# Kernel optimization log

Measured on AMD Instinct MI355X. Metric: run time of the kernel, lower is better.

The kernel has to match this reference:

```python
import jax, jax.numpy as jnp
import numpy as np

N_NODES = 100000
N_EDGES = 3200000
D_NODE = 16
D_EDGE = 8
D_HIDDEN = 16


def setup_inputs() -> dict:
    key = jax.random.key(0)
    ks = jax.random.split(key, 8)
    node_features = jax.random.normal(ks[0], (N_NODES, D_NODE), dtype=jnp.float32)
    edge_attr_e3nn = jax.random.normal(ks[1], (N_EDGES, D_EDGE), dtype=jnp.float32)
    node_attr_scalar_raw = jax.random.normal(ks[2], (N_NODES, 1), dtype=jnp.float32)
    W_msg_tp = jax.random.normal(ks[3], (D_NODE, D_EDGE, D_HIDDEN), dtype=jnp.float32)
    W_msg_lin = jax.random.normal(ks[4], (D_HIDDEN, D_HIDDEN), dtype=jnp.float32)
    W_upd_tp = jax.random.normal(ks[5], (D_NODE, D_HIDDEN, D_HIDDEN), dtype=jnp.float32)
    W_upd_lin = jax.random.normal(ks[6], (D_HIDDEN, D_NODE), dtype=jnp.float32)
    edge_index = jax.random.randint(ks[7], (2, N_EDGES), 0, N_NODES, dtype=jnp.int64)
    return {
        "node_features": node_features,
        "edge_attr_e3nn": edge_attr_e3nn,
        "node_attr_scalar_raw": node_attr_scalar_raw,
        "W_msg_tp": W_msg_tp,
        "W_msg_lin": W_msg_lin,
        "W_upd_tp": W_upd_tp,
        "W_upd_lin": W_upd_lin,
        "edge_index": edge_index,
    }


def reference(node_features, edge_attr_e3nn, node_attr_scalar_raw,
              W_msg_tp, W_msg_lin, W_upd_tp, W_upd_lin, edge_index):
    n_nodes = node_features.shape[0]
    row = edge_index[0]  # destination (aggregation target)
    col = edge_index[1]  # source (gathered neighbor)

    # fan-in normalizations (e3nn FullyConnectedTensorProduct / Linear convention)
    norm_msg_tp = 1.0 / np.float32(np.sqrt(D_NODE * D_EDGE))
    norm_upd_tp = 1.0 / np.float32(np.sqrt(D_NODE * D_HIDDEN))
    norm_lin = 1.0 / np.float32(np.sqrt(D_HIDDEN))

    # --- message step: gather -> bilinear TP -> gate -> linear ---
    x_j = node_features[col]                                   # [E, D_node]
    m = jnp.einsum('ei,ej,ijh->eh', x_j, edge_attr_e3nn, W_msg_tp) * norm_msg_tp
    m = jax.nn.silu(m)                                         # gate nonlinearity
    m = (m @ W_msg_lin) * norm_lin                             # [E, D_hidden]

    # --- scatter-sum aggregation into nodes ---
    agg = jax.ops.segment_sum(m, row, num_segments=n_nodes)    # [N, D_hidden]

    # --- update step: bilinear TP -> gate -> linear -> residual ---
    u = jnp.einsum('ni,nh,ihk->nk', node_features, agg, W_upd_tp) * norm_upd_tp
    u = jax.nn.silu(u)
    u = (u @ W_upd_lin) * norm_lin                             # [N, D_node]

    return node_features + u
```

## Files before the change

### kernel.cpp

```cpp
#include <hip/hip_runtime.h>
#include <math.h>

#define N_NODES_C 100000
#define N_EDGES_C 3200000

#define NORM_MSG_TP 0.08838834764831845f
#define NORM_UPD_TP 0.0625f
#define NORM_LIN    0.25f

typedef float f32x4 __attribute__((ext_vector_type(4)));
typedef short bf16x8 __attribute__((ext_vector_type(8)));
typedef int   int4v  __attribute__((ext_vector_type(4)));

__device__ __forceinline__ float silu_f(float v) {
  return v / (1.0f + __expf(-v));
}

__device__ __forceinline__ void atomic_add_hw(float* p, float v) {
  unsafeAtomicAdd(p, v);
}

__device__ __forceinline__ unsigned int bf16_bits(float f) {
  unsigned int b = __float_as_uint(f);
  return (b + 0x7fffu + ((b >> 16) & 1u)) >> 16;
}
__device__ __forceinline__ unsigned int pack_bf16x2(float lo, float hi) {
  return bf16_bits(lo) | (bf16_bits(hi) << 16);
}
__device__ __forceinline__ float unlo(unsigned int w) { return __uint_as_float(w << 16); }
__device__ __forceinline__ float unhi(unsigned int w) { return __uint_as_float(w & 0xffff0000u); }


__global__ __launch_bounds__(256) void zero_ints(int* __restrict__ p, int n) {
  int i = blockIdx.x * 256 + threadIdx.x;
  if (i < n) p[i] = 0;
}

__global__ __launch_bounds__(256) void hist_kernel(
    const int* __restrict__ row, int* __restrict__ cnt) {
  int e = blockIdx.x * 256 + threadIdx.x;
  atomicAdd(&cnt[row[e]], 1);
}

__global__ __launch_bounds__(256) void scan_block(
    const int* __restrict__ cnt, int* __restrict__ off, int* __restrict__ bsum, int n) {
  __shared__ int s[256];
  const int t = threadIdx.x;
  const int i = blockIdx.x * 256 + t;
  const int v = (i < n) ? cnt[i] : 0;
  s[t] = v;
  __syncthreads();
#pragma unroll
  for (int o = 1; o < 256; o <<= 1) {
    int tv = (t >= o) ? s[t - o] : 0;
    __syncthreads();
    s[t] += tv;
    __syncthreads();
  }
  if (i < n) off[i] = s[t] - v;
  if (t == 255) bsum[blockIdx.x] = s[255];
}

__global__ void scan_bsum(int* __restrict__ bsum, int nb) {
  __shared__ int s[512];
  const int t = threadIdx.x;
  const int v = (t < nb) ? bsum[t] : 0;
  s[t] = v;
  __syncthreads();
#pragma unroll
  for (int o = 1; o < 512; o <<= 1) {
    int tv = (t >= o) ? s[t - o] : 0;
    __syncthreads();
    s[t] += tv;
    __syncthreads();
  }
  if (t < nb) bsum[t] = s[t] - v;
}

__global__ __launch_bounds__(256) void scan_add(
    int* __restrict__ off, const int* __restrict__ bsum, int n, int total) {
  int i = blockIdx.x * 256 + threadIdx.x;
  if (i < n) off[i] += bsum[blockIdx.x];
  if (i == 0) off[n] = total;
}


__global__ __launch_bounds__(256) void xcast_kernel(
    const float* __restrict__ x, unsigned short* __restrict__ xb) {
  const int i = blockIdx.x * 256 + threadIdx.x;
  if (i < N_NODES_C * 2) {
    const float4 a = *reinterpret_cast<const float4*>(x + (size_t)i * 8);
    const float4 b = *reinterpret_cast<const float4*>(x + (size_t)i * 8 + 4);
    uint4 w;
    w.x = pack_bf16x2(a.x, a.y); w.y = pack_bf16x2(a.z, a.w);
    w.z = pack_bf16x2(b.x, b.y); w.w = pack_bf16x2(b.z, b.w);
    *reinterpret_cast<uint4*>(xb + (size_t)i * 8) = w;
  }
}


#define CLAIM_TILE(T, CC, PP) do {                                   \
    const int e_ = (T) * 16 + r;                                     \
    if (g == 0) {                                                    \
      CC = eidx[N_EDGES_C + e_];                                     \
      const int rd_ = eidx[e_];                                      \
      PP = off[rd_] + atomicSub(&cnt[rd_], 1) - 1;                   \
    }                                                                \
  } while (0)

#define GATH_TILE(T, CC, XH, F4) do {                                \
    const int e_ = (T) * 16 + r;                                     \
    const int c_ = __shfl(CC, r);                                    \
    if (g < 2) {                                                     \
      XH = *reinterpret_cast<const uint4*>(xb + (size_t)c_ * 16 + g * 8); \
      F4 = *reinterpret_cast<const float4*>(ea + (size_t)e_ * 8 + g * 4); \
    }                                                                \
  } while (0)

__global__ __launch_bounds__(256) void place4_kernel(
    const int*   __restrict__ eidx,
    const float* __restrict__ ea,
    const float* __restrict__ Wtp,
    const int*   __restrict__ off,
    int*         __restrict__ cnt,
    const unsigned short* __restrict__ xb,
    unsigned int* __restrict__ msort)
{
  __shared__ float sm[4][16][20];
  const int lane  = threadIdx.x & 63;
  const int wv    = threadIdx.x >> 6;
  const int r     = lane & 15;
  const int g     = lane >> 4;
  const int gsel  = g >> 1;
  const int ghalf = g & 1;

  bf16x8 bq[4];
#pragma unroll
  for (int q = 0; q < 4; ++q) {
#pragma unroll
    for (int t = 0; t < 8; ++t) {
      const float w = Wtp[(8 * ghalf + t) * 128 + (2 * q + gsel) * 16 + r];
      bq[q][t] = (short)bf16_bits(w);
    }
  }

  const int s = gridDim.x * 4;
  const int wid = blockIdx.x * 4 + wv;
  const int ntiles = N_EDGES_C / 16;

  int cc_a = 0, pp_a = 0, cc_b = 0, pp_b = 0;
  uint4 xh_a; xh_a.x = xh_a.y = xh_a.z = xh_a.w = 0;
  float4 f4_a = make_float4(0.f, 0.f, 0.f, 0.f);

  if (wid < ntiles)     CLAIM_TILE(wid, cc_a, pp_a);
  if (wid + s < ntiles) CLAIM_TILE(wid + s, cc_b, pp_b);
  if (wid < ntiles)     GATH_TILE(wid, cc_a, xh_a, f4_a);

  for (int t = wid; t < ntiles; t += s) {
    int cc_c = 0, pp_c = 0;
    if (t + 2 * s < ntiles) CLAIM_TILE(t + 2 * s, cc_c, pp_c);
    uint4 xh_b; xh_b.x = xh_b.y = xh_b.z = xh_b.w = 0;
    float4 f4_b = make_float4(0.f, 0.f, 0.f, 0.f);
    if (t + s < ntiles) GATH_TILE(t + s, cc_b, xh_b, f4_b);

    uint4 xh;
    xh.x = (unsigned)__shfl((int)xh_a.x, ghalf * 16 + r);
    xh.y = (unsigned)__shfl((int)xh_a.y, ghalf * 16 + r);
    xh.z = (unsigned)__shfl((int)xh_a.z, ghalf * 16 + r);
    xh.w = (unsigned)__shfl((int)xh_a.w, ghalf * 16 + r);
    float xf[8];
    xf[0] = unlo(xh.x); xf[1] = unhi(xh.x);
    xf[2] = unlo(xh.y); xf[3] = unhi(xh.y);
    xf[4] = unlo(xh.z); xf[5] = unhi(xh.z);
    xf[6] = unlo(xh.w); xf[7] = unhi(xh.w);
    const float a0 = __shfl(f4_a.x, r),      a1 = __shfl(f4_a.y, r);
    const float a2 = __shfl(f4_a.z, r),      a3 = __shfl(f4_a.w, r);
    const float b0 = __shfl(f4_a.x, 16 + r), b1 = __shfl(f4_a.y, 16 + r);
    const float b2 = __shfl(f4_a.z, 16 + r), b3 = __shfl(f4_a.w, 16 + r);
    float eq[4];
    eq[0] = gsel ? a1 : a0;  eq[1] = gsel ? a3 : a2;
    eq[2] = gsel ? b1 : b0;  eq[3] = gsel ? b3 : b2;

    f32x4 acc = {0.f, 0.f, 0.f, 0.f};
#pragma unroll
    for (int q = 0; q < 4; ++q) {
      const float e_ = eq[q];
      const unsigned u0 = __float_as_uint(xf[0] * e_) + 0x8000u;
      const unsigned u1 = __float_as_uint(xf[1] * e_) + 0x8000u;
      const unsigned u2 = __float_as_uint(xf[2] * e_) + 0x8000u;
      const unsigned u3 = __float_as_uint(xf[3] * e_) + 0x8000u;
      const unsigned u4 = __float_as_uint(xf[4] * e_) + 0x8000u;
      const unsigned u5 = __float_as_uint(xf[5] * e_) + 0x8000u;
      const unsigned u6 = __float_as_uint(xf[6] * e_) + 0x8000u;
      const unsigned u7 = __float_as_uint(xf[7] * e_) + 0x8000u;
      int4v iv;
      iv.x = (int)__builtin_amdgcn_perm(u1, u0, 0x07060302u);
      iv.y = (int)__builtin_amdgcn_perm(u3, u2, 0x07060302u);
      iv.z = (int)__builtin_amdgcn_perm(u5, u4, 0x07060302u);
      iv.w = (int)__builtin_amdgcn_perm(u7, u6, 0x07060302u);
      union { int4v i; bf16x8 h; } cv; cv.i = iv;
      acc = __builtin_amdgcn_mfma_f32_16x16x32_bf16(cv.h, bq[q], acc, 0, 0, 0);
    }

#pragma unroll
    for (int j2 = 0; j2 < 4; ++j2)
      sm[wv][g * 4 + j2][r] = silu_f(acc[j2] * NORM_MSG_TP);

    asm volatile("s_waitcnt lgkmcnt(0)" ::: "memory");
    __builtin_amdgcn_sched_barrier(0);

    const int rr  = lane >> 2;
    const int wsl = lane & 3;
    const float4 v4 = *reinterpret_cast<const float4*>(&sm[wv][rr][wsl * 4]);
    const int prr = __shfl(pp_a, rr);
    uint2 wout;
    wout.x = pack_bf16x2(v4.x, v4.y);
    wout.y = pack_bf16x2(v4.z, v4.w);
    *reinterpret_cast<uint2*>(&msort[(size_t)prr * 8 + wsl * 2]) = wout;

    pp_a = pp_b; xh_a = xh_b; f4_a = f4_b;
    cc_b = cc_c; pp_b = pp_c;
  }
}


__global__ __launch_bounds__(256) void agg3_kernel(
    const float* __restrict__ Wlin,
    const unsigned int* __restrict__ msort,
    const int*   __restrict__ off,
    float*       __restrict__ agg)
{
  __shared__ float sL[256];
  if (threadIdx.x < 256) sL[threadIdx.x] = Wlin[threadIdx.x];
  __syncthreads();

  const int slane = threadIdx.x & 15;
  const int n = blockIdx.x * 16 + (threadIdx.x >> 4);

  const int off0 = off[n];
  const int off1 = off[n + 1];

  float acc = 0.f;
  for (int p = off0; p < off1; ++p) {
    const unsigned int w = msort[(size_t)p * 8 + (slane >> 1)];
    acc += (slane & 1) ? unhi(w) : unlo(w);
  }

  float a = 0.f;
#pragma unroll
  for (int h = 0; h < 16; ++h) {
    const float v = __shfl(acc, h, 16);
    a = fmaf(v, sL[h * 16 + slane], a);
  }
  agg[(size_t)n * 16 + slane] = a * NORM_LIN;
}


__global__ __launch_bounds__(256) void tbuild_kernel(
    const float* __restrict__ x, const float* __restrict__ Wtp,
    uint4* __restrict__ Tb)
{
  __shared__ float sWT[16 * 132];
  for (int idx = threadIdx.x; idx < 2048; idx += 256) {
    const int i = idx >> 7, j = (idx >> 4) & 7, h = idx & 15;
    sWT[h * 132 + i * 8 + j] = Wtp[idx];
  }
  __syncthreads();

  const int slane = threadIdx.x & 15;
  const int n = blockIdx.x * 16 + (threadIdx.x >> 4);

  float xr[16];
  const float4* xp = reinterpret_cast<const float4*>(x + (size_t)n * 16);
#pragma unroll
  for (int q = 0; q < 4; ++q) {
    float4 v = xp[q];
    xr[q*4+0] = v.x; xr[q*4+1] = v.y; xr[q*4+2] = v.z; xr[q*4+3] = v.w;
  }

  float t[8];
#pragma unroll
  for (int j = 0; j < 8; ++j) t[j] = 0.f;
#pragma unroll
  for (int i = 0; i < 16; ++i) {
    const float xi = xr[i];
    const float4 wa = *reinterpret_cast<const float4*>(&sWT[slane * 132 + i * 8]);
    const float4 wb = *reinterpret_cast<const float4*>(&sWT[slane * 132 + i * 8 + 4]);
    t[0] = fmaf(xi, wa.x, t[0]); t[1] = fmaf(xi, wa.y, t[1]);
    t[2] = fmaf(xi, wa.z, t[2]); t[3] = fmaf(xi, wa.w, t[3]);
    t[4] = fmaf(xi, wb.x, t[4]); t[5] = fmaf(xi, wb.y, t[5]);
    t[6] = fmaf(xi, wb.z, t[6]); t[7] = fmaf(xi, wb.w, t[7]);
  }
  uint4 w;
  w.x = pack_bf16x2(t[0], t[1]);
  w.y = pack_bf16x2(t[2], t[3]);
  w.z = pack_bf16x2(t[4], t[5]);
  w.w = pack_bf16x2(t[6], t[7]);
  Tb[(size_t)n * 16 + slane] = w;
}

__global__ __launch_bounds__(256) void place_kernel(
    const int* __restrict__ eidx, const float* __restrict__ ea,
    const int* __restrict__ off, int* __restrict__ cnt,
    int* __restrict__ colp, uint4* __restrict__ eab) {
  int e = blockIdx.x * 256 + threadIdx.x;
  const int r = eidx[e];
  const int old = atomicSub(&cnt[r], 1);
  const int p = off[r] + old - 1;
  colp[p] = eidx[N_EDGES_C + e];
  const float4* ep = reinterpret_cast<const float4*>(ea + (size_t)e * 8);
  const float4 a = ep[0];
  const float4 b = ep[1];
  uint4 w;
  w.x = pack_bf16x2(a.x, a.y);
  w.y = pack_bf16x2(a.z, a.w);
  w.z = pack_bf16x2(b.x, b.y);
  w.w = pack_bf16x2(b.z, b.w);
  eab[p] = w;
}

__global__ __launch_bounds__(256) void agg2_kernel(
    const float* __restrict__ Wlin, const int* __restrict__ colp,
    const uint4* __restrict__ eab, const uint4* __restrict__ Tb,
    const int* __restrict__ off, float* __restrict__ agg)
{
  __shared__ float sL[256];
  if (threadIdx.x < 256) sL[threadIdx.x] = Wlin[threadIdx.x];
  __syncthreads();

  const int slane = threadIdx.x & 15;
  const int n = blockIdx.x * 16 + (threadIdx.x >> 4);

  const int off0 = off[n];
  const int off1 = off[n + 1];

  float acc = 0.f;
#pragma unroll 2
  for (int p = off0; p < off1; ++p) {
    const int c = colp[p];
    const uint4 tw = Tb[(size_t)c * 16 + slane];
    const uint4 ew = eab[p];
    float m;
    m  = unlo(ew.x) * unlo(tw.x);
    m  = fmaf(unhi(ew.x), unhi(tw.x), m);
    m  = fmaf(unlo(ew.y), unlo(tw.y), m);
    m  = fmaf(unhi(ew.y), unhi(tw.y), m);
    m  = fmaf(unlo(ew.z), unlo(tw.z), m);
    m  = fmaf(unhi(ew.z), unhi(tw.z), m);
    m  = fmaf(unlo(ew.w), unlo(tw.w), m);
    m  = fmaf(unhi(ew.w), unhi(tw.w), m);
    acc += silu_f(m * NORM_MSG_TP);
  }

  float a = 0.f;
#pragma unroll
  for (int h = 0; h < 16; ++h) {
    const float v = __shfl(acc, h, 16);
    a = fmaf(v, sL[h * 16 + slane], a);
  }
  agg[(size_t)n * 16 + slane] = a * NORM_LIN;
}


__global__ __launch_bounds__(256) void node_kernel(
    const float* __restrict__ x, const float* __restrict__ agg,
    const float* __restrict__ Wtp, const float* __restrict__ Wlin,
    float* __restrict__ out)
{
  __shared__ float sW[4096];
  __shared__ float sL[256];
  for (int t = threadIdx.x; t < 4096; t += 256) sW[t] = Wtp[t];
  sL[threadIdx.x] = Wlin[threadIdx.x];
  __syncthreads();

  const long n = (long)blockIdx.x * 256 + threadIdx.x;
  if (n >= N_NODES_C) return;

  float xr[16], ar[16];
  const float4* xp = reinterpret_cast<const float4*>(x + (size_t)n * 16);
  const float4* ap = reinterpret_cast<const float4*>(agg + (size_t)n * 16);
#pragma unroll
  for (int q = 0; q < 4; ++q) {
    float4 v = xp[q];
    xr[q*4+0] = v.x; xr[q*4+1] = v.y; xr[q*4+2] = v.z; xr[q*4+3] = v.w;
    float4 w = ap[q];
    ar[q*4+0] = w.x; ar[q*4+1] = w.y; ar[q*4+2] = w.z; ar[q*4+3] = w.w;
  }
  float u[16];
#pragma unroll
  for (int k = 0; k < 16; ++k) u[k] = 0.f;
#pragma unroll
  for (int i = 0; i < 16; ++i) {
#pragma unroll
    for (int h = 0; h < 16; ++h) {
      const float p = xr[i] * ar[h];
      const float* w = &sW[(i*16 + h) * 16];
#pragma unroll
      for (int k = 0; k < 16; ++k) u[k] = fmaf(p, w[k], u[k]);
    }
  }
  float g[16];
#pragma unroll
  for (int k = 0; k < 16; ++k) g[k] = silu_f(u[k] * NORM_UPD_TP);
  float res[16];
#pragma unroll
  for (int k2 = 0; k2 < 16; ++k2) {
    float a = 0.f;
#pragma unroll
    for (int k = 0; k < 16; ++k) a = fmaf(g[k], sL[k*16 + k2], a);
    res[k2] = xr[k2] + a * NORM_LIN;
  }
  float4* op = reinterpret_cast<float4*>(out + (size_t)n * 16);
#pragma unroll
  for (int q = 0; q < 4; ++q)
    op[q] = make_float4(res[q*4+0], res[q*4+1], res[q*4+2], res[q*4+3]);
}


__global__ void zero_f4(float4* __restrict__ p, int n4) {
  int i = blockIdx.x * blockDim.x + threadIdx.x;
  if (i < n4) p[i] = make_float4(0.f, 0.f, 0.f, 0.f);
}

#define EPT 2
__global__ __launch_bounds__(256) void edge_kernel(
    const float* __restrict__ x, const float* __restrict__ ea,
    const float* __restrict__ Wtp, const float* __restrict__ Wlin,
    const int* __restrict__ eidx, float* __restrict__ agg)
{
  __shared__ float sW[2048];
  __shared__ float sL[256];
  for (int t = threadIdx.x; t < 2048; t += 256) sW[t] = Wtp[t];
  sL[threadIdx.x] = Wlin[threadIdx.x];
  __syncthreads();
  const long e0 = ((long)blockIdx.x * 256 + threadIdx.x) * EPT;
  float xr[EPT][16], er[EPT][8];
  int rw[EPT];
#pragma unroll
  for (int e = 0; e < EPT; ++e) {
    const long ei = e0 + e;
    const int c = eidx[N_EDGES_C + ei];
    rw[e] = eidx[ei];
    const float4* xp = reinterpret_cast<const float4*>(x + (size_t)c * 16);
#pragma unroll
    for (int q = 0; q < 4; ++q) {
      float4 v = xp[q];
      xr[e][q*4+0] = v.x; xr[e][q*4+1] = v.y; xr[e][q*4+2] = v.z; xr[e][q*4+3] = v.w;
    }
    const float4* ep = reinterpret_cast<const float4*>(ea + (size_t)ei * 8);
#pragma unroll
    for (int q = 0; q < 2; ++q) {
      float4 v = ep[q];
      er[e][q*4+0] = v.x; er[e][q*4+1] = v.y; er[e][q*4+2] = v.z; er[e][q*4+3] = v.w;
    }
  }
  float m[EPT][16];
#pragma unroll
  for (int e = 0; e < EPT; ++e)
#pragma unroll
    for (int h = 0; h < 16; ++h) m[e][h] = 0.f;
#pragma unroll
  for (int i = 0; i < 16; ++i) {
#pragma unroll
    for (int j = 0; j < 8; ++j) {
      float p[EPT];
#pragma unroll
      for (int e = 0; e < EPT; ++e) p[e] = xr[e][i] * er[e][j];
      const float* w = &sW[(i*8 + j) * 16];
#pragma unroll
      for (int h = 0; h < 16; ++h) {
        const float wv = w[h];
#pragma unroll
        for (int e = 0; e < EPT; ++e) m[e][h] = fmaf(p[e], wv, m[e][h]);
      }
    }
  }
#pragma unroll
  for (int e = 0; e < EPT; ++e) {
    float g[16];
#pragma unroll
    for (int h = 0; h < 16; ++h) g[h] = silu_f(m[e][h] * NORM_MSG_TP);
    float* ap = agg + (size_t)rw[e] * 16;
#pragma unroll
    for (int h2 = 0; h2 < 16; ++h2) {
      float a = 0.f;
#pragma unroll
      for (int h = 0; h < 16; ++h) a = fmaf(g[h], sL[h*16 + h2], a);
      atomic_add_hw(ap + h2, a * NORM_LIN);
    }
  }
}


extern "C" void kernel_launch(void* const* d_in, const int* in_sizes, int n_in,
                              void* d_out, int out_size, void* d_ws, size_t ws_size,
                              hipStream_t stream) {
  const float* node_features = (const float*)d_in[0];
  const float* edge_attr     = (const float*)d_in[1];
  const float* W_msg_tp      = (const float*)d_in[3];
  const float* W_msg_lin     = (const float*)d_in[4];
  const float* W_upd_tp      = (const float*)d_in[5];
  const float* W_upd_lin     = (const float*)d_in[6];
  const int*   edge_index    = (const int*)d_in[7];
  float* out = (float*)d_out;
  char* ws = (char*)d_ws;

  const int NB_N = (N_NODES_C + 255) / 256;
  const int NB_E = N_EDGES_C / 256;
  const int NB_G = N_NODES_C / 16;

  const size_t A_OFF  = 0;
  const size_t A_CNT  = 400128;
  const size_t A_BSUM = 800256;
  const size_t A_MSORT= 802304;
  const size_t A_XB   = A_MSORT + 102400000;
  const size_t A_AGG  = A_XB + 3200000;
  const size_t A_NEED = A_AGG + 6400000;

  const size_t B_OFF  = 0;
  const size_t B_CNT  = 400128;
  const size_t B_BSUM = 800256;
  const size_t B_COLP = 804352;
  const size_t B_EAB  = B_COLP + 12800000;
  const size_t B_T    = B_EAB + 51200000;
  const size_t B_AGG  = B_T + 25600000;
  const size_t B_NEED = B_AGG + 6400000;

  if (ws_size >= A_NEED) {
    int*   off   = (int*)(ws + A_OFF);
    int*   cnt   = (int*)(ws + A_CNT);
    int*   bsum  = (int*)(ws + A_BSUM);
    unsigned int* msort = (unsigned int*)(ws + A_MSORT);
    unsigned short* xb  = (unsigned short*)(ws + A_XB);
    float* agg   = (float*)(ws + A_AGG);

    hipLaunchKernelGGL(zero_ints, dim3(NB_N), dim3(256), 0, stream, cnt, N_NODES_C);
    hipLaunchKernelGGL(hist_kernel, dim3(NB_E), dim3(256), 0, stream, edge_index, cnt);
    hipLaunchKernelGGL(scan_block, dim3(NB_N), dim3(256), 0, stream,
                       cnt, off, bsum, N_NODES_C);
    hipLaunchKernelGGL(scan_bsum, dim3(1), dim3(512), 0, stream, bsum, NB_N);
    hipLaunchKernelGGL(scan_add, dim3(NB_N), dim3(256), 0, stream,
                       off, bsum, N_NODES_C, N_EDGES_C);
    hipLaunchKernelGGL(xcast_kernel, dim3((N_NODES_C * 2 + 255) / 256), dim3(256),
                       0, stream, node_features, xb);
    hipLaunchKernelGGL(place4_kernel, dim3(2048), dim3(256), 0, stream,
                       edge_index, edge_attr, W_msg_tp, off, cnt, xb, msort);
    hipLaunchKernelGGL(agg3_kernel, dim3(NB_G), dim3(256), 0, stream,
                       W_msg_lin, msort, off, agg);
    hipLaunchKernelGGL(node_kernel, dim3(NB_N), dim3(256), 0, stream,
                       node_features, agg, W_upd_tp, W_upd_lin, out);
  } else if (ws_size >= B_NEED) {
    int*   off  = (int*)(ws + B_OFF);
    int*   cnt  = (int*)(ws + B_CNT);
    int*   bsum = (int*)(ws + B_BSUM);
    int*   colp = (int*)(ws + B_COLP);
    uint4* eab  = (uint4*)(ws + B_EAB);
    uint4* Tb   = (uint4*)(ws + B_T);
    float* agg  = (float*)(ws + B_AGG);

    hipLaunchKernelGGL(zero_ints, dim3(NB_N), dim3(256), 0, stream, cnt, N_NODES_C);
    hipLaunchKernelGGL(hist_kernel, dim3(NB_E), dim3(256), 0, stream, edge_index, cnt);
    hipLaunchKernelGGL(scan_block, dim3(NB_N), dim3(256), 0, stream,
                       cnt, off, bsum, N_NODES_C);
    hipLaunchKernelGGL(scan_bsum, dim3(1), dim3(512), 0, stream, bsum, NB_N);
    hipLaunchKernelGGL(scan_add, dim3(NB_N), dim3(256), 0, stream,
                       off, bsum, N_NODES_C, N_EDGES_C);
    hipLaunchKernelGGL(place_kernel, dim3(NB_E), dim3(256), 0, stream,
                       edge_index, edge_attr, off, cnt, colp, eab);
    hipLaunchKernelGGL(tbuild_kernel, dim3(NB_G), dim3(256), 0, stream,
                       node_features, W_msg_tp, Tb);
    hipLaunchKernelGGL(agg2_kernel, dim3(NB_G), dim3(256), 0, stream,
                       W_msg_lin, colp, eab, Tb, off, agg);
    hipLaunchKernelGGL(node_kernel, dim3(NB_N), dim3(256), 0, stream,
                       node_features, agg, W_upd_tp, W_upd_lin, out);
  } else {
    float* agg = (float*)ws;
    const int n4 = N_NODES_C * 16 / 4;
    hipLaunchKernelGGL(zero_f4, dim3((n4 + 255) / 256), dim3(256), 0, stream,
                       (float4*)agg, n4);
    hipLaunchKernelGGL(edge_kernel, dim3(N_EDGES_C / (256 * EPT)), dim3(256), 0, stream,
                       node_features, edge_attr, W_msg_tp, W_msg_lin, edge_index, agg);
    hipLaunchKernelGGL(node_kernel, dim3(NB_N), dim3(256), 0, stream,
                       node_features, agg, W_upd_tp, W_upd_lin, out);
  }
}
```

Measured before the change: 381.7 us.

## Write messages in edge order and gather via permutation during aggregation

Splits the edge placement out into its own kernel that builds a CSR permutation of edge ids. The message kernel now writes bf16 messages contiguously in edge order instead of scattering them to sorted positions. The aggregation kernel gathers messages indirectly through the permutation, unrolled by four. This swaps scattered 16-byte writes for coalesced writes, at the cost of an extra kernel, a 12.8 MB permutation array, and random reads during aggregation.

```diff
diff --git a/kernel.cpp b/kernel.cpp
--- a/kernel.cpp
+++ b/kernel.cpp
@@ -82,6 +82,15 @@
   int i = blockIdx.x * 256 + threadIdx.x;
   if (i < n) off[i] += bsum[blockIdx.x];
   if (i == 0) off[n] = total;
+}
+
+__global__ __launch_bounds__(256) void placeP_kernel(
+    const int* __restrict__ eidx, const int* __restrict__ off,
+    int* __restrict__ cnt, int* __restrict__ perm) {
+  int e = blockIdx.x * 256 + threadIdx.x;
+  const int r = eidx[e];
+  const int p = off[r] + atomicSub(&cnt[r], 1) - 1;
+  perm[p] = e;
 }
 
 
@@ -99,13 +108,8 @@
 }
 
 
-#define CLAIM_TILE(T, CC, PP) do {                                   \
-    const int e_ = (T) * 16 + r;                                     \
-    if (g == 0) {                                                    \
-      CC = eidx[N_EDGES_C + e_];                                     \
-      const int rd_ = eidx[e_];                                      \
-      PP = off[rd_] + atomicSub(&cnt[rd_], 1) - 1;                   \
-    }                                                                \
+#define COLS_TILE(T, CC) do {                                        \
+    if (g == 0) CC = eidx[N_EDGES_C + (T) * 16 + r];                 \
   } while (0)
 
 #define GATH_TILE(T, CC, XH, F4) do {                                \
@@ -117,14 +121,12 @@
     }                                                                \
   } while (0)
 
-__global__ __launch_bounds__(256) void place4_kernel(
+__global__ __launch_bounds__(256) void msg_kernel(
     const int*   __restrict__ eidx,
     const float* __restrict__ ea,
     const float* __restrict__ Wtp,
-    const int*   __restrict__ off,
-    int*         __restrict__ cnt,
     const unsigned short* __restrict__ xb,
-    unsigned int* __restrict__ msort)
+    unsigned int* __restrict__ msgb)
 {
   __shared__ float sm[4][16][20];
   const int lane  = threadIdx.x & 63;
@@ -148,17 +150,17 @@
   const int wid = blockIdx.x * 4 + wv;
   const int ntiles = N_EDGES_C / 16;
 
-  int cc_a = 0, pp_a = 0, cc_b = 0, pp_b = 0;
+  int cc_a = 0, cc_b = 0;
   uint4 xh_a; xh_a.x = xh_a.y = xh_a.z = xh_a.w = 0;
   float4 f4_a = make_float4(0.f, 0.f, 0.f, 0.f);
 
-  if (wid < ntiles)     CLAIM_TILE(wid, cc_a, pp_a);
-  if (wid + s < ntiles) CLAIM_TILE(wid + s, cc_b, pp_b);
+  if (wid < ntiles)     COLS_TILE(wid, cc_a);
+  if (wid + s < ntiles) COLS_TILE(wid + s, cc_b);
   if (wid < ntiles)     GATH_TILE(wid, cc_a, xh_a, f4_a);
 
   for (int t = wid; t < ntiles; t += s) {
-    int cc_c = 0, pp_c = 0;
-    if (t + 2 * s < ntiles) CLAIM_TILE(t + 2 * s, cc_c, pp_c);
+    int cc_c = 0;
+    if (t + 2 * s < ntiles) COLS_TILE(t + 2 * s, cc_c);
     uint4 xh_b; xh_b.x = xh_b.y = xh_b.z = xh_b.w = 0;
     float4 f4_b = make_float4(0.f, 0.f, 0.f, 0.f);
     if (t + s < ntiles) GATH_TILE(t + s, cc_b, xh_b, f4_b);
@@ -212,21 +214,20 @@
     const int rr  = lane >> 2;
     const int wsl = lane & 3;
     const float4 v4 = *reinterpret_cast<const float4*>(&sm[wv][rr][wsl * 4]);
-    const int prr = __shfl(pp_a, rr);
     uint2 wout;
     wout.x = pack_bf16x2(v4.x, v4.y);
     wout.y = pack_bf16x2(v4.z, v4.w);
-    *reinterpret_cast<uint2*>(&msort[(size_t)prr * 8 + wsl * 2]) = wout;
-
-    pp_a = pp_b; xh_a = xh_b; f4_a = f4_b;
-    cc_b = cc_c; pp_b = pp_c;
-  }
-}
-
-
-__global__ __launch_bounds__(256) void agg3_kernel(
+    *reinterpret_cast<uint2*>(&msgb[(size_t)(t * 16 + rr) * 8 + wsl * 2]) = wout;
+
+    xh_a = xh_b; f4_a = f4_b; cc_b = cc_c;
+  }
+}
+
+
+__global__ __launch_bounds__(256) void agg4_kernel(
     const float* __restrict__ Wlin,
-    const unsigned int* __restrict__ msort,
+    const int*   __restrict__ perm,
+    const unsigned int* __restrict__ msgb,
     const int*   __restrict__ off,
     float*       __restrict__ agg)
 {
@@ -235,14 +236,25 @@
   __syncthreads();
 
   const int slane = threadIdx.x & 15;
+  const int wsel  = slane >> 1;
   const int n = blockIdx.x * 16 + (threadIdx.x >> 4);
 
   const int off0 = off[n];
   const int off1 = off[n + 1];
 
   float acc = 0.f;
-  for (int p = off0; p < off1; ++p) {
-    const unsigned int w = msort[(size_t)p * 8 + (slane >> 1)];
+  int p = off0;
+  for (; p + 3 < off1; p += 4) {
+    const int e0 = perm[p], e1 = perm[p + 1], e2 = perm[p + 2], e3 = perm[p + 3];
+    const unsigned w0 = msgb[(size_t)e0 * 8 + wsel];
+    const unsigned w1 = msgb[(size_t)e1 * 8 + wsel];
+    const unsigned w2 = msgb[(size_t)e2 * 8 + wsel];
+    const unsigned w3 = msgb[(size_t)e3 * 8 + wsel];
+    if (slane & 1) acc += unhi(w0) + unhi(w1) + unhi(w2) + unhi(w3);
+    else           acc += unlo(w0) + unlo(w1) + unlo(w2) + unlo(w3);
+  }
+  for (; p < off1; ++p) {
+    const unsigned w = msgb[(size_t)perm[p] * 8 + wsel];
     acc += (slane & 1) ? unhi(w) : unlo(w);
   }
 
@@ -512,8 +524,9 @@
   const size_t A_OFF  = 0;
   const size_t A_CNT  = 400128;
   const size_t A_BSUM = 800256;
-  const size_t A_MSORT= 802304;
-  const size_t A_XB   = A_MSORT + 102400000;
+  const size_t A_PERM = 802304;
+  const size_t A_MSGB = A_PERM + 12800000;
+  const size_t A_XB   = A_MSGB + 102400000;
   const size_t A_AGG  = A_XB + 3200000;
   const size_t A_NEED = A_AGG + 6400000;
 
@@ -530,8 +543,9 @@
     int*   off   = (int*)(ws + A_OFF);
     int*   cnt   = (int*)(ws + A_CNT);
     int*   bsum  = (int*)(ws + A_BSUM);
-    unsigned int* msort = (unsigned int*)(ws + A_MSORT);
-    unsigned short* xb  = (unsigned short*)(ws + A_XB);
+    int*   perm  = (int*)(ws + A_PERM);
+    unsigned int* msgb = (unsigned int*)(ws + A_MSGB);
+    unsigned short* xb = (unsigned short*)(ws + A_XB);
     float* agg   = (float*)(ws + A_AGG);
 
     hipLaunchKernelGGL(zero_ints, dim3(NB_N), dim3(256), 0, stream, cnt, N_NODES_C);
@@ -541,12 +555,14 @@
     hipLaunchKernelGGL(scan_bsum, dim3(1), dim3(512), 0, stream, bsum, NB_N);
     hipLaunchKernelGGL(scan_add, dim3(NB_N), dim3(256), 0, stream,
                        off, bsum, N_NODES_C, N_EDGES_C);
+    hipLaunchKernelGGL(placeP_kernel, dim3(NB_E), dim3(256), 0, stream,
+                       edge_index, off, cnt, perm);
     hipLaunchKernelGGL(xcast_kernel, dim3((N_NODES_C * 2 + 255) / 256), dim3(256),
                        0, stream, node_features, xb);
-    hipLaunchKernelGGL(place4_kernel, dim3(2048), dim3(256), 0, stream,
-                       edge_index, edge_attr, W_msg_tp, off, cnt, xb, msort);
-    hipLaunchKernelGGL(agg3_kernel, dim3(NB_G), dim3(256), 0, stream,
-                       W_msg_lin, msort, off, agg);
+    hipLaunchKernelGGL(msg_kernel, dim3(2048), dim3(256), 0, stream,
+                       edge_index, edge_attr, W_msg_tp, xb, msgb);
+    hipLaunchKernelGGL(agg4_kernel, dim3(NB_G), dim3(256), 0, stream,
+                       W_msg_lin, perm, msgb, off, agg);
     hipLaunchKernelGGL(node_kernel, dim3(NB_N), dim3(256), 0, stream,
                        node_features, agg, W_upd_tp, W_upd_lin, out);
   } else if (ws_size >= B_NEED) {
```

Result: slower. 538.3 us (+41.0%).

## Record per-edge slot in histogram pass and use nontemporal stores for sorted messages

Applied to the files above, without the earlier changes.

The histogram kernel now saves the atomicAdd return value as each edge's position within its destination bucket. The placement kernel then computes its output slot as off[row]+pos with a plain load, with no second atomicSub pass on the counters. Sorted message writes become 64-bit nontemporal stores to limit cache pollution. The cost is an extra 12.8MB pos array written and read back. The agg buffer aliases pos and is reused after placement; in path B, colp is scratch for pos and is overwritten later.

```diff
diff --git a/kernel.cpp b/kernel.cpp
--- a/kernel.cpp
+++ b/kernel.cpp
@@ -37,9 +37,9 @@
 }
 
 __global__ __launch_bounds__(256) void hist_kernel(
-    const int* __restrict__ row, int* __restrict__ cnt) {
+    const int* __restrict__ row, int* __restrict__ cnt, int* __restrict__ pos) {
   int e = blockIdx.x * 256 + threadIdx.x;
-  atomicAdd(&cnt[row[e]], 1);
+  pos[e] = atomicAdd(&cnt[row[e]], 1);
 }
 
 __global__ __launch_bounds__(256) void scan_block(
@@ -103,8 +103,7 @@
     const int e_ = (T) * 16 + r;                                     \
     if (g == 0) {                                                    \
       CC = eidx[N_EDGES_C + e_];                                     \
-      const int rd_ = eidx[e_];                                      \
-      PP = off[rd_] + atomicSub(&cnt[rd_], 1) - 1;                   \
+      PP = off[eidx[e_]] + pos[e_];                                  \
     }                                                                \
   } while (0)
 
@@ -122,7 +121,7 @@
     const float* __restrict__ ea,
     const float* __restrict__ Wtp,
     const int*   __restrict__ off,
-    int*         __restrict__ cnt,
+    const int*   __restrict__ pos,
     const unsigned short* __restrict__ xb,
     unsigned int* __restrict__ msort)
 {
@@ -213,10 +212,11 @@
     const int wsl = lane & 3;
     const float4 v4 = *reinterpret_cast<const float4*>(&sm[wv][rr][wsl * 4]);
     const int prr = __shfl(pp_a, rr);
-    uint2 wout;
-    wout.x = pack_bf16x2(v4.x, v4.y);
-    wout.y = pack_bf16x2(v4.z, v4.w);
-    *reinterpret_cast<uint2*>(&msort[(size_t)prr * 8 + wsl * 2]) = wout;
+    const unsigned long long wout =
+        (unsigned long long)pack_bf16x2(v4.x, v4.y) |
+        ((unsigned long long)pack_bf16x2(v4.z, v4.w) << 32);
+    __builtin_nontemporal_store(
+        wout, reinterpret_cast<unsigned long long*>(&msort[(size_t)prr * 8 + wsl * 2]));
 
     pp_a = pp_b; xh_a = xh_b; f4_a = f4_b;
     cc_b = cc_c; pp_b = pp_c;
@@ -512,10 +512,10 @@
   const size_t A_OFF  = 0;
   const size_t A_CNT  = 400128;
   const size_t A_BSUM = 800256;
-  const size_t A_MSORT= 802304;
+  const size_t A_POS  = 802304;
+  const size_t A_MSORT= A_POS + 12800000;
   const size_t A_XB   = A_MSORT + 102400000;
-  const size_t A_AGG  = A_XB + 3200000;
-  const size_t A_NEED = A_AGG + 6400000;
+  const size_t A_NEED = A_XB + 3200000;
 
   const size_t B_OFF  = 0;
   const size_t B_CNT  = 400128;
@@ -530,12 +530,14 @@
     int*   off   = (int*)(ws + A_OFF);
     int*   cnt   = (int*)(ws + A_CNT);
     int*   bsum  = (int*)(ws + A_BSUM);
+    int*   pos   = (int*)(ws + A_POS);
     unsigned int* msort = (unsigned int*)(ws + A_MSORT);
     unsigned short* xb  = (unsigned short*)(ws + A_XB);
-    float* agg   = (float*)(ws + A_AGG);
+    float* agg   = (float*)(ws + A_POS);
 
     hipLaunchKernelGGL(zero_ints, dim3(NB_N), dim3(256), 0, stream, cnt, N_NODES_C);
-    hipLaunchKernelGGL(hist_kernel, dim3(NB_E), dim3(256), 0, stream, edge_index, cnt);
+    hipLaunchKernelGGL(hist_kernel, dim3(NB_E), dim3(256), 0, stream,
+                       edge_index, cnt, pos);
     hipLaunchKernelGGL(scan_block, dim3(NB_N), dim3(256), 0, stream,
                        cnt, off, bsum, N_NODES_C);
     hipLaunchKernelGGL(scan_bsum, dim3(1), dim3(512), 0, stream, bsum, NB_N);
@@ -544,7 +546,7 @@
     hipLaunchKernelGGL(xcast_kernel, dim3((N_NODES_C * 2 + 255) / 256), dim3(256),
                        0, stream, node_features, xb);
     hipLaunchKernelGGL(place4_kernel, dim3(2048), dim3(256), 0, stream,
-                       edge_index, edge_attr, W_msg_tp, off, cnt, xb, msort);
+                       edge_index, edge_attr, W_msg_tp, off, pos, xb, msort);
     hipLaunchKernelGGL(agg3_kernel, dim3(NB_G), dim3(256), 0, stream,
                        W_msg_lin, msort, off, agg);
     hipLaunchKernelGGL(node_kernel, dim3(NB_N), dim3(256), 0, stream,
@@ -559,7 +561,8 @@
     float* agg  = (float*)(ws + B_AGG);
 
     hipLaunchKernelGGL(zero_ints, dim3(NB_N), dim3(256), 0, stream, cnt, N_NODES_C);
-    hipLaunchKernelGGL(hist_kernel, dim3(NB_E), dim3(256), 0, stream, edge_index, cnt);
+    hipLaunchKernelGGL(hist_kernel, dim3(NB_E), dim3(256), 0, stream,
+                       edge_index, cnt, colp );
     hipLaunchKernelGGL(scan_block, dim3(NB_N), dim3(256), 0, stream,
                        cnt, off, bsum, N_NODES_C);
     hipLaunchKernelGGL(scan_bsum, dim3(1), dim3(512), 0, stream, bsum, NB_N);
```

Result: no change. 374.9 us (-1.8%).
